# Kernel tuning notes

Hardware: AMD Instinct MI355X
Metric: run time of the kernel (lower is better)

## Reference

```python
import jax, jax.numpy as jnp
import numpy as np

B = 8192
TEXT_DIM = 2048
GRAPH_DIM = 1024
OUT_DIM = 1024
C = 2048  # common_dim = max(text_dim, graph_dim)
H = 16    # num_heads
LN_EPS = 1e-5


def _linear(x, W, b):
    # torch nn.Linear: y = x @ W.T + b, W: [out, in]
    return x @ W.T + b


def _mha(q, k, v, Wqkv, bqkv, Wo, bo):
    # Faithful to torch nn.MultiheadAttention (batch_first, eval mode).
    # Wqkv: [3C, C], bqkv: [3C], Wo: [C, C], bo: [C]
    Bq, S, _ = q.shape
    D = C // H
    Wq, Wk, Wv = Wqkv[:C], Wqkv[C:2 * C], Wqkv[2 * C:]
    bq, bk, bv = bqkv[:C], bqkv[C:2 * C], bqkv[2 * C:]
    qh = _linear(q, Wq, bq).reshape(Bq, S, H, D).transpose(0, 2, 1, 3)  # [B,H,S,D]
    kh = _linear(k, Wk, bk).reshape(Bq, S, H, D).transpose(0, 2, 1, 3)
    vh = _linear(v, Wv, bv).reshape(Bq, S, H, D).transpose(0, 2, 1, 3)
    scores = jnp.einsum('bhqd,bhkd->bhqk', qh, kh) / jnp.sqrt(jnp.asarray(D, qh.dtype))
    attn = jax.nn.softmax(scores, axis=-1)
    out = jnp.einsum('bhqk,bhkd->bhqd', attn, vh)
    out = out.transpose(0, 2, 1, 3).reshape(Bq, S, C)
    return _linear(out, Wo, bo)


def _layernorm(x, w, b):
    mu = jnp.mean(x, axis=-1, keepdims=True)
    var = jnp.mean(jnp.square(x - mu), axis=-1, keepdims=True)
    return (x - mu) * jax.lax.rsqrt(var + LN_EPS) * w + b


def setup_inputs() -> dict:
    key = jax.random.key(0)
    ks = jax.random.split(key, 16)
    s = 0.02
    return {
        'text_embeddings': jax.random.normal(ks[0], (B, TEXT_DIM), jnp.float32),
        'graph_embeddings': jax.random.normal(ks[1], (B, GRAPH_DIM), jnp.float32),
        'Wt': jax.random.normal(ks[2], (C, TEXT_DIM), jnp.float32) * s,
        'bt': jnp.zeros((C,), jnp.float32),
        'Wg': jax.random.normal(ks[3], (C, GRAPH_DIM), jnp.float32) * s,
        'bg': jnp.zeros((C,), jnp.float32),
        'Wqkv_s': jax.random.normal(ks[4], (3 * C, C), jnp.float32) * s,
        'bqkv_s': jnp.zeros((3 * C,), jnp.float32),
        'Wo_s': jax.random.normal(ks[5], (C, C), jnp.float32) * s,
        'bo_s': jnp.zeros((C,), jnp.float32),
        'Wqkv_c': jax.random.normal(ks[6], (3 * C, C), jnp.float32) * s,
        'bqkv_c': jnp.zeros((3 * C,), jnp.float32),
        'Wo_c': jax.random.normal(ks[7], (C, C), jnp.float32) * s,
        'bo_c': jnp.zeros((C,), jnp.float32),
        'ln_w': jnp.ones((C,), jnp.float32),
        'ln_b': jnp.zeros((C,), jnp.float32),
        'Wout': jax.random.normal(ks[8], (OUT_DIM, C), jnp.float32) * s,
        'bout': jnp.zeros((OUT_DIM,), jnp.float32),
    }


def reference(text_embeddings, graph_embeddings, Wt, bt, Wg, bg,
              Wqkv_s, bqkv_s, Wo_s, bo_s, Wqkv_c, bqkv_c, Wo_c, bo_c,
              ln_w, ln_b, Wout, bout):
    text_proj = _linear(text_embeddings, Wt, bt)    # [B, C]
    graph_proj = _linear(graph_embeddings, Wg, bg)  # [B, C]
    stacked = jnp.stack([text_proj, graph_proj], axis=1)  # [B, 2, C]
    attn_out = _mha(stacked, stacked, stacked, Wqkv_s, bqkv_s, Wo_s, bo_s)
    attn_out = _layernorm(attn_out, ln_w, ln_b)
    cross = _mha(attn_out, stacked, stacked, Wqkv_c, bqkv_c, Wo_c, bo_c)
    attn_out = attn_out + cross
    fused = jnp.mean(attn_out, axis=1)  # [B, C]
    return _linear(fused, Wout, bout)   # [B, OUT_DIM]
```

## Files before the change

kernel.cpp:

```cpp
#include <hip/hip_runtime.h>
#include <cstdio>

typedef unsigned short u16;
typedef float f32x4 __attribute__((ext_vector_type(4)));
typedef short s16x8 __attribute__((ext_vector_type(8)));

__device__ __forceinline__ u16 f2bf(float x) {
    unsigned u = __float_as_uint(x);
    u += 0x7fffu + ((u >> 16) & 1u);
    return (u16)(u >> 16);
}
__device__ __forceinline__ unsigned pack2(float a, float b) {
    return (unsigned)f2bf(a) | ((unsigned)f2bf(b) << 16);
}
__device__ __forceinline__ void unpack2(unsigned u, float& lo, float& hi) {
    lo = __uint_as_float(u << 16);
    hi = __uint_as_float(u & 0xffff0000u);
}

__device__ __forceinline__ void gl2lds16(const u16* g, u16* l) {
    __builtin_amdgcn_global_load_lds(
        (const __attribute__((address_space(1))) void*)g,
        (__attribute__((address_space(3))) void*)l, 16, 0, 0);
}

__device__ __forceinline__ uint4 ld8(const u16* p) { return *(const uint4*)p; }
__device__ __forceinline__ uint4 ld8(const float* p) {
    float4 a = ((const float4*)p)[0];
    float4 b = ((const float4*)p)[1];
    uint4 r;
    r.x = pack2(a.x, a.y);
    r.y = pack2(a.z, a.w);
    r.z = pack2(b.x, b.y);
    r.w = pack2(b.z, b.w);
    return r;
}

__global__ __launch_bounds__(256) void cast_f32_bf16(const float* __restrict__ x,
                                                     u16* __restrict__ y, int n4) {
    int i = blockIdx.x * 256 + threadIdx.x;
    if (i >= n4) return;
    float4 v = ((const float4*)x)[i];
    uint2 r;
    r.x = pack2(v.x, v.y);
    r.y = pack2(v.z, v.w);
    ((uint2*)y)[i] = r;
}

template <typename TA, typename TB, bool OUT_BF16>
__global__ __launch_bounds__(256) void gemm_bt(const TA* __restrict__ A,
                                               const TB* __restrict__ B,
                                               const float* __restrict__ bias,
                                               void* __restrict__ Cout,
                                               int K, int ldc) {
    __shared__ __align__(16) u16 As[128 * 32];
    __shared__ __align__(16) u16 Bs[128 * 32];

    const int tid = threadIdx.x;
    const int lane = tid & 63;
    const int wave = tid >> 6;
    const int wm = wave >> 1;
    const int wn = wave & 1;
    const size_t bm = (size_t)blockIdx.y * 128;
    const size_t bn = (size_t)blockIdx.x * 128;

    f32x4 acc[4][4];
#pragma unroll
    for (int i = 0; i < 4; ++i)
#pragma unroll
        for (int j = 0; j < 4; ++j) acc[i][j] = (f32x4)0.f;

    const int srow = tid >> 2;
    const int scol = (tid & 3) << 3;
    const TA* Ag = A + (bm + (size_t)srow) * K + scol;
    const TB* Bg = B + (bn + (size_t)srow) * K + scol;
    const size_t rstep = (size_t)64 * K;

    uint4 a0 = ld8(Ag);
    uint4 a1 = ld8(Ag + rstep);
    uint4 b0 = ld8(Bg);
    uint4 b1 = ld8(Bg + rstep);

    const int lrow = lane & 15;
    const int lk = (lane >> 4) << 3;

    const int niter = K >> 5;
    for (int t = 0; t < niter; ++t) {
        __syncthreads();
        *(uint4*)&As[srow * 32 + scol] = a0;
        *(uint4*)&As[(64 + srow) * 32 + scol] = a1;
        *(uint4*)&Bs[srow * 32 + scol] = b0;
        *(uint4*)&Bs[(64 + srow) * 32 + scol] = b1;
        __syncthreads();
        if (t + 1 < niter) {
            const int k0 = (t + 1) << 5;
            a0 = ld8(Ag + k0);
            a1 = ld8(Ag + rstep + k0);
            b0 = ld8(Bg + k0);
            b1 = ld8(Bg + rstep + k0);
        }
        s16x8 af[4], bfr[4];
#pragma unroll
        for (int i = 0; i < 4; ++i)
            af[i] = *(const s16x8*)&As[(wm * 64 + i * 16 + lrow) * 32 + lk];
#pragma unroll
        for (int j = 0; j < 4; ++j)
            bfr[j] = *(const s16x8*)&Bs[(wn * 64 + j * 16 + lrow) * 32 + lk];
#pragma unroll
        for (int i = 0; i < 4; ++i)
#pragma unroll
            for (int j = 0; j < 4; ++j)
                acc[i][j] = __builtin_amdgcn_mfma_f32_16x16x32_bf16(
                    af[i], bfr[j], acc[i][j], 0, 0, 0);
    }

    const size_t crow0 = bm + wm * 64 + ((lane >> 4) << 2);
    const int ccol0 = (int)bn + wn * 64 + (lane & 15);
#pragma unroll
    for (int i = 0; i < 4; ++i) {
#pragma unroll
        for (int j = 0; j < 4; ++j) {
            const int col = ccol0 + j * 16;
            const float bv = bias[col];
            const size_t base = (crow0 + (size_t)i * 16) * (size_t)ldc + col;
#pragma unroll
            for (int r = 0; r < 4; ++r) {
                const float v = acc[i][j][r] + bv;
                if (OUT_BF16)
                    ((u16*)Cout)[base + (size_t)r * ldc] = f2bf(v);
                else
                    ((float*)Cout)[base + (size_t)r * ldc] = v;
            }
        }
    }
}

template <bool OUT_BF16>
__global__ __launch_bounds__(256) void gemm_async(const u16* __restrict__ A, int lda,
                                                  const u16* __restrict__ B,
                                                  const float* __restrict__ bias,
                                                  void* __restrict__ Cout,
                                                  int K, int ldc) {
    __shared__ __align__(16) u16 As[128 * 32];
    __shared__ __align__(16) u16 Bs[128 * 32];

    const int tid = threadIdx.x;
    const int lane = tid & 63;
    const int wave = tid >> 6;
    const int wm = wave >> 1;
    const int wn = wave & 1;
    const size_t bm = (size_t)blockIdx.y * 128;
    const size_t bn = (size_t)blockIdx.x * 128;

    f32x4 acc[4][4];
#pragma unroll
    for (int i = 0; i < 4; ++i)
#pragma unroll
        for (int j = 0; j < 4; ++j) acc[i][j] = (f32x4)0.f;

    const int srow = tid >> 2;
    const int scol = (tid & 3) << 3;
    const u16* Ag = A + (bm + (size_t)srow) * (size_t)lda + scol;
    const u16* Bg = B + (bn + (size_t)srow) * (size_t)K + scol;
    const size_t rA = (size_t)64 * lda;
    const size_t rB = (size_t)64 * K;
    u16* lA0 = &As[tid * 8];
    u16* lA1 = &As[2048 + tid * 8];
    u16* lB0 = &Bs[tid * 8];
    u16* lB1 = &Bs[2048 + tid * 8];

    const int lrow = lane & 15;
    const int lk = (lane >> 4) << 3;

    const int niter = K >> 5;
    for (int t = 0; t < niter; ++t) {
        __syncthreads();
        gl2lds16(Ag, lA0);
        gl2lds16(Ag + rA, lA1);
        gl2lds16(Bg, lB0);
        gl2lds16(Bg + rB, lB1);
        Ag += 32;
        Bg += 32;
        __syncthreads();
        s16x8 af[4], bfr[4];
#pragma unroll
        for (int i = 0; i < 4; ++i)
            af[i] = *(const s16x8*)&As[(wm * 64 + i * 16 + lrow) * 32 + lk];
#pragma unroll
        for (int j = 0; j < 4; ++j)
            bfr[j] = *(const s16x8*)&Bs[(wn * 64 + j * 16 + lrow) * 32 + lk];
#pragma unroll
        for (int i = 0; i < 4; ++i)
#pragma unroll
            for (int j = 0; j < 4; ++j)
                acc[i][j] = __builtin_amdgcn_mfma_f32_16x16x32_bf16(
                    af[i], bfr[j], acc[i][j], 0, 0, 0);
    }

    const size_t crow0 = bm + wm * 64 + ((lane >> 4) << 2);
    const int ccol0 = (int)bn + wn * 64 + (lane & 15);
#pragma unroll
    for (int i = 0; i < 4; ++i) {
#pragma unroll
        for (int j = 0; j < 4; ++j) {
            const int col = ccol0 + j * 16;
            const float bv = bias[col];
            const size_t base = (crow0 + (size_t)i * 16) * (size_t)ldc + col;
#pragma unroll
            for (int r = 0; r < 4; ++r) {
                const float v = acc[i][j][r] + bv;
                if (OUT_BF16)
                    ((u16*)Cout)[base + (size_t)r * ldc] = f2bf(v);
                else
                    ((float*)Cout)[base + (size_t)r * ldc] = v;
            }
        }
    }
}

#define STG_A02(v)                                                            \
    do {                                                                      \
        gl2lds16(aG + (size_t)(v) * 64, &As[(v) & 1][tid * 8]);               \
        gl2lds16(aG + 2 * a64 + (size_t)(v) * 64,                             \
                 &As[(v) & 1][8192 + tid * 8]);                               \
    } while (0)
#define STG_A13(v)                                                            \
    do {                                                                      \
        gl2lds16(aG + a64 + (size_t)(v) * 64, &As[(v) & 1][4096 + tid * 8]);  \
        gl2lds16(aG + 3 * a64 + (size_t)(v) * 64,                             \
                 &As[(v) & 1][12288 + tid * 8]);                              \
    } while (0)
#define STG_B01(v)                                                            \
    do {                                                                      \
        gl2lds16(bG + (size_t)(v) * 64, &Bs[(v) & 1][tid * 8]);               \
        gl2lds16(bG + b64 + (size_t)(v) * 64, &Bs[(v) & 1][4096 + tid * 8]);  \
    } while (0)
#define STG_B23(v)                                                            \
    do {                                                                      \
        gl2lds16(bG + 2 * b64 + (size_t)(v) * 64,                             \
                 &Bs[(v) & 1][8192 + tid * 8]);                               \
        gl2lds16(bG + 3 * b64 + (size_t)(v) * 64,                             \
                 &Bs[(v) & 1][12288 + tid * 8]);                              \
    } while (0)
#define RD_AF(buf, mh, m)                                                     \
    do {                                                                      \
        const u16* p_ = &As[buf][aRow + ((mh) * 64 + (m) * 16) * 64];         \
        aF[m][0] = *(const s16x8*)(p_ + aK0);                                 \
        aF[m][1] = *(const s16x8*)(p_ + aK1);                                 \
    } while (0)
#define RD_B(buf, nh, dst)                                                    \
    do {                                                                      \
        _Pragma("unroll") for (int n_ = 0; n_ < 2; ++n_) {                    \
            const u16* p_ = &Bs[buf][bRow + ((nh) * 32 + n_ * 16) * 64];      \
            dst[n_][0] = *(const s16x8*)(p_ + aK0);                           \
            dst[n_][1] = *(const s16x8*)(p_ + aK1);                           \
        }                                                                     \
    } while (0)
#define MFMA4(ar, bv, ci, cj)                                                 \
    do {                                                                      \
        acc[ci][cj] = __builtin_amdgcn_mfma_f32_16x16x32_bf16(                \
            (ar)[0], (bv)[0], acc[ci][cj], 0, 0, 0);                          \
        acc[ci][cj] = __builtin_amdgcn_mfma_f32_16x16x32_bf16(                \
            (ar)[1], (bv)[1], acc[ci][cj], 0, 0, 0);                          \
    } while (0)

#define TILEW(u, SA13, S2, RDN, V2S, V4S)                                     \
    do {                                                                      \
        const int cur = (u) & 1, oth = cur ^ 1;                               \
                                                          \
        if (SA13) STG_A13((u) + 1);                                           \
        RD_B(cur, 1, b1);                                                     \
        __builtin_amdgcn_s_setprio(1);                                        \
        _Pragma("unroll") for (int m = 0; m < 4; ++m) {                       \
            MFMA4(aF[m], b0[0], m, 0);                                        \
            MFMA4(aF[m], b0[1], m, 1);                                        \
        }                                                                     \
        __builtin_amdgcn_s_setprio(0);                                        \
        asm volatile("s_waitcnt " V2S ::: "memory");                          \
        __builtin_amdgcn_s_barrier();                                         \
                                  \
        if (S2) STG_A02((u) + 2);                                             \
        __builtin_amdgcn_s_setprio(1);                                        \
        _Pragma("unroll") for (int m = 0; m < 4; ++m) {                       \
            MFMA4(aF[m], b1[0], m, 2);                                        \
            MFMA4(aF[m], b1[1], m, 3);                                        \
            RD_AF(cur, 1, m);                                                 \
        }                                                                     \
        __builtin_amdgcn_s_setprio(0);                                        \
        __builtin_amdgcn_s_barrier();                                         \
                                                          \
        if (S2) STG_B01((u) + 2);                                             \
        __builtin_amdgcn_s_setprio(1);                                        \
        _Pragma("unroll") for (int m = 0; m < 4; ++m) {                       \
            MFMA4(aF[m], b1[0], 4 + m, 2);                                    \
            MFMA4(aF[m], b1[1], 4 + m, 3);                                    \
        }                                                                     \
        __builtin_amdgcn_s_setprio(0);                                        \
        asm volatile("s_waitcnt " V4S ::: "memory");                          \
        __builtin_amdgcn_s_barrier();                                         \
                         \
        if (S2) STG_B23((u) + 2);                                             \
        __builtin_amdgcn_s_setprio(1);                                        \
        _Pragma("unroll") for (int m = 0; m < 4; ++m) {                       \
            MFMA4(aF[m], b0[0], 4 + m, 0);                                    \
            MFMA4(aF[m], b0[1], 4 + m, 1);                                    \
            if (RDN) RD_AF(oth, 0, m);                                        \
        }                                                                     \
        __builtin_amdgcn_s_setprio(0);                                        \
        if (RDN) RD_B(oth, 0, b0);                                            \
        __builtin_amdgcn_s_barrier();                                         \
    } while (0)

template <bool OUT_BF16>
__global__ __launch_bounds__(512, 2) void gemm8(const u16* __restrict__ A, int lda,
                                                const u16* __restrict__ B,
                                                const float* __restrict__ bias,
                                                void* __restrict__ Cout,
                                                int K, int ldc) {
    __shared__ __align__(16) u16 As[2][16384];
    __shared__ __align__(16) u16 Bs[2][16384];

    const int tid = threadIdx.x;
    const int lane = tid & 63;
    const int wave = tid >> 6;
    const int wm = wave >> 2;
    const int wn = wave & 3;

    const unsigned nwg = gridDim.x * gridDim.y;
    const unsigned orig = blockIdx.y * gridDim.x + blockIdx.x;
    const unsigned q = nwg >> 3, r = nwg & 7u;
    const unsigned xcd = orig & 7u, idx = orig >> 3;
    const unsigned wg =
        (xcd < r ? xcd * (q + 1) : r * (q + 1) + (xcd - r) * q) + idx;
    const size_t bm = (size_t)(wg / gridDim.x) * 256;
    const size_t bn = (size_t)(wg % gridDim.x) * 256;

    f32x4 acc[8][4];
#pragma unroll
    for (int i = 0; i < 8; ++i)
#pragma unroll
        for (int j = 0; j < 4; ++j) acc[i][j] = (f32x4)0.f;

    const int strow = tid >> 3;
    const int ssw = ((tid & 7) << 3) ^ ((strow & 7) << 3);
    const u16* aG = A + (bm + (size_t)strow) * (size_t)lda + ssw;
    const u16* bG = B + (bn + (size_t)strow) * (size_t)K + ssw;
    const size_t a64 = (size_t)64 * lda;
    const size_t b64 = (size_t)64 * K;

    const int lrow = lane & 15;
    const int hi8 = (lane >> 4) << 3;
    const int fswz = (lrow & 7) << 3;
    const int aK0 = hi8 ^ fswz;
    const int aK1 = (32 + hi8) ^ fswz;
    const int aRow = (wm * 128 + lrow) * 64;
    const int bRow = (wn * 64 + lrow) * 64;

    s16x8 aF[4][2], b0[2][2], b1[2][2];

    const int NT = K >> 6;

    STG_A02(0);
    STG_A13(0);
    STG_B01(0);
    STG_B23(0);
    STG_A02(1);
    STG_B01(1);
    STG_B23(1);
    asm volatile("s_waitcnt vmcnt(6)" ::: "memory");
    __builtin_amdgcn_s_barrier();
#pragma unroll
    for (int m = 0; m < 4; ++m) RD_AF(0, 0, m);
    RD_B(0, 0, b0);

    for (int u = 0; u < NT - 2; ++u)
        TILEW(u, 1, 1, 1, "vmcnt(8)", "vmcnt(6)");
    TILEW(NT - 2, 1, 0, 1, "vmcnt(8)", "vmcnt(2)");
    TILEW(NT - 1, 0, 0, 0, "vmcnt(0)", "vmcnt(0)");

    const size_t crow0 = bm + wm * 128 + ((lane >> 4) << 2);
    const int ccol0 = (int)bn + wn * 64 + (lane & 15);
#pragma unroll
    for (int im = 0; im < 8; ++im) {
#pragma unroll
        for (int in = 0; in < 4; ++in) {
            const int col = ccol0 + in * 16;
            const float bv = bias[col];
            const size_t base = (crow0 + (size_t)im * 16) * (size_t)ldc + col;
#pragma unroll
            for (int r = 0; r < 4; ++r) {
                const float v = acc[im][in][r] + bv;
                if (OUT_BF16)
                    ((u16*)Cout)[base + (size_t)r * ldc] = f2bf(v);
                else
                    ((float*)Cout)[base + (size_t)r * ldc] = v;
            }
        }
    }
}

#undef STG_A02
#undef STG_A13
#undef STG_B01
#undef STG_B23
#undef RD_AF
#undef RD_B
#undef MFMA4
#undef TILEW

__device__ __forceinline__ void dot8(uint4 a, uint4 b, float& acc) {
    const unsigned* pa = (const unsigned*)&a;
    const unsigned* pb = (const unsigned*)&b;
#pragma unroll
    for (int i = 0; i < 4; ++i) {
        float alo, ahi, blo, bhi;
        unpack2(pa[i], alo, ahi);
        unpack2(pb[i], blo, bhi);
        acc += alo * blo + ahi * bhi;
    }
}

__global__ __launch_bounds__(256) void attn2(u16* __restrict__ qkv) {
    const int gid = blockIdx.x * 256 + threadIdx.x;
    const int b = gid >> 4;
    const int h = gid & 15;
    u16* base = qkv + (size_t)(2 * b) * 6144 + h * 128;
    float s00 = 0.f, s01 = 0.f, s10 = 0.f, s11 = 0.f;
#pragma unroll 4
    for (int c = 0; c < 128; c += 8) {
        uint4 q0 = *(const uint4*)(base + c);
        uint4 q1 = *(const uint4*)(base + 6144 + c);
        uint4 k0 = *(const uint4*)(base + 2048 + c);
        uint4 k1 = *(const uint4*)(base + 8192 + c);
        dot8(q0, k0, s00);
        dot8(q0, k1, s01);
        dot8(q1, k0, s10);
        dot8(q1, k1, s11);
    }
    const float scale = 0.0883883476483184f;
    s00 *= scale; s01 *= scale; s10 *= scale; s11 *= scale;
    const float m0 = fmaxf(s00, s01), m1 = fmaxf(s10, s11);
    const float e00 = __expf(s00 - m0), e01 = __expf(s01 - m0);
    const float e10 = __expf(s10 - m1), e11 = __expf(s11 - m1);
    const float r0 = 1.f / (e00 + e01), r1 = 1.f / (e10 + e11);
    const float p00 = e00 * r0, p01 = e01 * r0;
    const float p10 = e10 * r1, p11 = e11 * r1;

#pragma unroll 4
    for (int c = 0; c < 128; c += 8) {
        uint4 v0 = *(const uint4*)(base + 4096 + c);
        uint4 v1 = *(const uint4*)(base + 10240 + c);
        const unsigned* p0w = (const unsigned*)&v0;
        const unsigned* p1w = (const unsigned*)&v1;
        uint4 r0v, r1v;
        unsigned* q0w = (unsigned*)&r0v;
        unsigned* q1w = (unsigned*)&r1v;
#pragma unroll
        for (int i = 0; i < 4; ++i) {
            float v0lo, v0hi, v1lo, v1hi;
            unpack2(p0w[i], v0lo, v0hi);
            unpack2(p1w[i], v1lo, v1hi);
            q0w[i] = pack2(p00 * v0lo + p01 * v1lo, p00 * v0hi + p01 * v1hi);
            q1w[i] = pack2(p10 * v0lo + p11 * v1lo, p10 * v0hi + p11 * v1hi);
        }
        *(uint4*)(base + c) = r0v;
        *(uint4*)(base + 6144 + c) = r1v;
    }
}

__global__ __launch_bounds__(256) void ln_k(const u16* __restrict__ x, int ldx,
                                            const float* __restrict__ w,
                                            const float* __restrict__ bb,
                                            u16* __restrict__ y) {
    __shared__ float red[8];
    const int row = blockIdx.x;
    const int tid = threadIdx.x;
    const uint4 v = ((const uint4*)(x + (size_t)row * ldx))[tid];
    const unsigned* pw = (const unsigned*)&v;
    float f[8];
#pragma unroll
    for (int i = 0; i < 4; ++i) unpack2(pw[i], f[2 * i], f[2 * i + 1]);
    float s = 0.f, q = 0.f;
#pragma unroll
    for (int i = 0; i < 8; ++i) {
        s += f[i];
        q += f[i] * f[i];
    }
#pragma unroll
    for (int off = 32; off > 0; off >>= 1) {
        s += __shfl_down(s, off);
        q += __shfl_down(q, off);
    }
    if ((tid & 63) == 0) {
        red[tid >> 6] = s;
        red[4 + (tid >> 6)] = q;
    }
    __syncthreads();
    s = red[0] + red[1] + red[2] + red[3];
    q = red[4] + red[5] + red[6] + red[7];
    const float mu = s * (1.f / 2048.f);
    const float var = q * (1.f / 2048.f) - mu * mu;
    const float rstd = rsqrtf(var + 1e-5f);
    const float4 w0 = ((const float4*)w)[2 * tid];
    const float4 w1 = ((const float4*)w)[2 * tid + 1];
    const float4 b0 = ((const float4*)bb)[2 * tid];
    const float4 b1 = ((const float4*)bb)[2 * tid + 1];
    const float wv[8] = {w0.x, w0.y, w0.z, w0.w, w1.x, w1.y, w1.z, w1.w};
    const float bv[8] = {b0.x, b0.y, b0.z, b0.w, b1.x, b1.y, b1.z, b1.w};
    uint4 o;
    unsigned* po = (unsigned*)&o;
#pragma unroll
    for (int i = 0; i < 4; ++i) {
        float lo = (f[2 * i] - mu) * rstd * wv[2 * i] + bv[2 * i];
        float hi = (f[2 * i + 1] - mu) * rstd * wv[2 * i + 1] + bv[2 * i + 1];
        po[i] = pack2(lo, hi);
    }
    ((uint4*)(y + (size_t)row * 2048))[tid] = o;
}

__global__ __launch_bounds__(256) void mean_res(const u16* __restrict__ ln,
                                                const u16* __restrict__ co,
                                                u16* __restrict__ fused) {
    const int gid = blockIdx.x * 256 + threadIdx.x;
    const int b = gid >> 8;
    const int c8 = gid & 255;
    const uint4 l0 = ((const uint4*)(ln + (size_t)(2 * b) * 2048))[c8];
    const uint4 l1 = ((const uint4*)(ln + (size_t)(2 * b + 1) * 2048))[c8];
    const uint4 c0 = ((const uint4*)(co + (size_t)(2 * b) * 6144))[c8];
    const uint4 c1 = ((const uint4*)(co + (size_t)(2 * b + 1) * 6144))[c8];
    const unsigned* pl0 = (const unsigned*)&l0;
    const unsigned* pl1 = (const unsigned*)&l1;
    const unsigned* pc0 = (const unsigned*)&c0;
    const unsigned* pc1 = (const unsigned*)&c1;
    uint4 o;
    unsigned* po = (unsigned*)&o;
#pragma unroll
    for (int i = 0; i < 4; ++i) {
        float a_lo, a_hi, b_lo, b_hi, c_lo, c_hi, d_lo, d_hi;
        unpack2(pl0[i], a_lo, a_hi);
        unpack2(pl1[i], b_lo, b_hi);
        unpack2(pc0[i], c_lo, c_hi);
        unpack2(pc1[i], d_lo, d_hi);
        po[i] = pack2(0.5f * (a_lo + c_lo + b_lo + d_lo),
                      0.5f * (a_hi + c_hi + b_hi + d_hi));
    }
    ((uint4*)(fused + (size_t)b * 12288))[c8] = o;
}

extern "C" void kernel_launch(void* const* d_in, const int* in_sizes, int n_in,
                              void* d_out, int out_size, void* d_ws, size_t ws_size,
                              hipStream_t stream) {
    (void)in_sizes; (void)n_in; (void)out_size;
    const float* text   = (const float*)d_in[0];
    const float* graph  = (const float*)d_in[1];
    const float* Wt     = (const float*)d_in[2];
    const float* bt     = (const float*)d_in[3];
    const float* Wg     = (const float*)d_in[4];
    const float* bg     = (const float*)d_in[5];
    const float* Wqkv_s = (const float*)d_in[6];
    const float* bqkv_s = (const float*)d_in[7];
    const float* Wo_s   = (const float*)d_in[8];
    const float* bo_s   = (const float*)d_in[9];
    const float* Wqkv_c = (const float*)d_in[10];
    const float* bqkv_c = (const float*)d_in[11];
    const float* Wo_c   = (const float*)d_in[12];
    const float* bo_c   = (const float*)d_in[13];
    const float* ln_w   = (const float*)d_in[14];
    const float* ln_b   = (const float*)d_in[15];
    const float* Wout   = (const float*)d_in[16];
    const float* bout   = (const float*)d_in[17];
    float* out = (float*)d_out;

    char* ws = (char*)d_ws;
    u16* wQs  = (u16*)ws;
    u16* wQc  = wQs + 12582912ull;
    u16* wOs  = wQc + 12582912ull;
    u16* wOc  = wOs + 4194304ull;
    u16* wWt  = wOc + 4194304ull;
    u16* wWg  = wWt + 4194304ull;
    u16* wOut = wWg + 2097152ull;
    const size_t WB = 83886080ull;

    size_t CH = 8192;
    while (CH > 128 && WB + 40960ull * CH > ws_size) CH >>= 1;
    fprintf(stderr, "[kernel_launch] ws_size=%zu need=%zu CH=%zu\n",
            ws_size, WB + 40960ull * CH, CH);
    if (WB + 40960ull * CH > ws_size || d_ws == nullptr) return;

    const size_t T = 2 * CH;
    char* ca = ws + WB;
    u16* stacked_c = (u16*)ca;
    u16* ln_c      = (u16*)(ca + 4096 * T);
    u16* qkv_c     = (u16*)(ca + 8192 * T);

    auto cast = [&](const float* x, u16* y, size_t n) {
        int n4 = (int)(n >> 2);
        cast_f32_bf16<<<(n4 + 255) / 256, 256, 0, stream>>>(x, y, n4);
    };
    cast(Wqkv_s, wQs, 12582912ull);
    cast(Wqkv_c, wQc, 12582912ull);
    cast(Wo_s, wOs, 4194304ull);
    cast(Wo_c, wOc, 4194304ull);
    cast(Wt, wWt, 4194304ull);
    cast(Wg, wWg, 2097152ull);
    cast(Wout, wOut, 2097152ull);

    const dim3 blk(256);
    const dim3 blk8(512);
    const unsigned gy  = (unsigned)(CH / 128);
    const unsigned g8  = (unsigned)(T / 256);

    for (size_t c0 = 0; c0 < 8192; c0 += CH) {
        gemm_bt<float, u16, true><<<dim3(16, gy), blk, 0, stream>>>(
            text + c0 * 2048, wWt, bt, stacked_c, 2048, 4096);
        gemm_bt<float, u16, true><<<dim3(16, gy), blk, 0, stream>>>(
            graph + c0 * 1024, wWg, bg, stacked_c + 2048, 1024, 4096);
        gemm8<true><<<dim3(24, g8), blk8, 0, stream>>>(
            stacked_c, 2048, wQs, bqkv_s, qkv_c, 2048, 6144);
        attn2<<<(unsigned)(CH / 16), blk, 0, stream>>>(qkv_c);
        gemm8<true><<<dim3(8, g8), blk8, 0, stream>>>(
            qkv_c, 6144, wOs, bo_s, qkv_c + 4096, 2048, 6144);
        ln_k<<<(unsigned)T, blk, 0, stream>>>(qkv_c + 4096, 6144, ln_w, ln_b, ln_c);
        gemm8<true><<<dim3(8, g8), blk8, 0, stream>>>(
            ln_c, 2048, wQc, bqkv_c, qkv_c, 2048, 6144);
        gemm8<true><<<dim3(16, g8), blk8, 0, stream>>>(
            stacked_c, 2048, wQc + 2048ull * 2048, bqkv_c + 2048,
            qkv_c + 2048, 2048, 6144);
        attn2<<<(unsigned)(CH / 16), blk, 0, stream>>>(qkv_c);
        gemm8<true><<<dim3(8, g8), blk8, 0, stream>>>(
            qkv_c, 6144, wOc, bo_c, qkv_c + 4096, 2048, 6144);
        mean_res<<<(unsigned)CH, blk, 0, stream>>>(ln_c, qkv_c + 4096, qkv_c);
        gemm_async<false><<<dim3(8, gy), blk, 0, stream>>>(
            qkv_c, 12288, wOut, bout, out + c0 * 1024, 2048, 1024);
    }
}
```

Before: 1.955 ms.

## Restructure GEMM main loop into four barrier-separated LDS-read/MFMA phases

Replaces the interleaved TILEW schedule, which overlapped LDS fragment reads with MFMAs and prefetched the next tile's fragments, with a TILE4 scheme. Each of the four quadrants now reads its fragments, waits on lgkmcnt(0), then runs its MFMAs behind sched_barriers. Global-to-LDS staging of A is moved to only one tile ahead and the prologue stages less up front. The aim is to simplify the schedule and cut dependence stalls. The cost is that LDS read latency is no longer hidden behind MFMAs and there are more barriers per tile.

```diff
diff --git a/kernel.cpp b/kernel.cpp
--- a/kernel.cpp
+++ b/kernel.cpp
@@ -256,58 +256,56 @@
             dst[n_][1] = *(const s16x8*)(p_ + aK1);                           \
         }                                                                     \
     } while (0)
-#define MFMA4(ar, bv, ci, cj)                                                 \
-    do {                                                                      \
-        acc[ci][cj] = __builtin_amdgcn_mfma_f32_16x16x32_bf16(                \
-            (ar)[0], (bv)[0], acc[ci][cj], 0, 0, 0);                          \
-        acc[ci][cj] = __builtin_amdgcn_mfma_f32_16x16x32_bf16(                \
-            (ar)[1], (bv)[1], acc[ci][cj], 0, 0, 0);                          \
-    } while (0)
-
-#define TILEW(u, SA13, S2, RDN, V2S, V4S)                                     \
-    do {                                                                      \
-        const int cur = (u) & 1, oth = cur ^ 1;                               \
-                                                          \
-        if (SA13) STG_A13((u) + 1);                                           \
-        RD_B(cur, 1, b1);                                                     \
+#define MFMA_Q(mh, nh, bf)                                                    \
+    do {                                                                      \
         __builtin_amdgcn_s_setprio(1);                                        \
-        _Pragma("unroll") for (int m = 0; m < 4; ++m) {                       \
-            MFMA4(aF[m], b0[0], m, 0);                                        \
-            MFMA4(aF[m], b0[1], m, 1);                                        \
+        _Pragma("unroll") for (int m = 0; m < 4; ++m)                         \
+            _Pragma("unroll") for (int n = 0; n < 2; ++n) {                   \
+            acc[(mh)*4 + m][(nh)*2 + n] =                                     \
+                __builtin_amdgcn_mfma_f32_16x16x32_bf16(                      \
+                    aF[m][0], bf[n][0], acc[(mh)*4 + m][(nh)*2 + n], 0, 0, 0);\
+            acc[(mh)*4 + m][(nh)*2 + n] =                                     \
+                __builtin_amdgcn_mfma_f32_16x16x32_bf16(                      \
+                    aF[m][1], bf[n][1], acc[(mh)*4 + m][(nh)*2 + n], 0, 0, 0);\
         }                                                                     \
         __builtin_amdgcn_s_setprio(0);                                        \
-        asm volatile("s_waitcnt " V2S ::: "memory");                          \
-        __builtin_amdgcn_s_barrier();                                         \
-                                  \
-        if (S2) STG_A02((u) + 2);                                             \
-        __builtin_amdgcn_s_setprio(1);                                        \
-        _Pragma("unroll") for (int m = 0; m < 4; ++m) {                       \
-            MFMA4(aF[m], b1[0], m, 2);                                        \
-            MFMA4(aF[m], b1[1], m, 3);                                        \
-            RD_AF(cur, 1, m);                                                 \
-        }                                                                     \
-        __builtin_amdgcn_s_setprio(0);                                        \
-        __builtin_amdgcn_s_barrier();                                         \
-                                                          \
-        if (S2) STG_B01((u) + 2);                                             \
-        __builtin_amdgcn_s_setprio(1);                                        \
-        _Pragma("unroll") for (int m = 0; m < 4; ++m) {                       \
-            MFMA4(aF[m], b1[0], 4 + m, 2);                                    \
-            MFMA4(aF[m], b1[1], 4 + m, 3);                                    \
-        }                                                                     \
-        __builtin_amdgcn_s_setprio(0);                                        \
-        asm volatile("s_waitcnt " V4S ::: "memory");                          \
-        __builtin_amdgcn_s_barrier();                                         \
-                         \
-        if (S2) STG_B23((u) + 2);                                             \
-        __builtin_amdgcn_s_setprio(1);                                        \
-        _Pragma("unroll") for (int m = 0; m < 4; ++m) {                       \
-            MFMA4(aF[m], b0[0], 4 + m, 0);                                    \
-            MFMA4(aF[m], b0[1], 4 + m, 1);                                    \
-            if (RDN) RD_AF(oth, 0, m);                                        \
-        }                                                                     \
-        __builtin_amdgcn_s_setprio(0);                                        \
-        if (RDN) RD_B(oth, 0, b0);                                            \
+    } while (0)
+
+#define TILE4(u, DO_A, DO_B, W2S, W4S)                                        \
+    do {                                                                      \
+        const int cur = (u) & 1;                                              \
+                                                                      \
+        _Pragma("unroll") for (int m = 0; m < 4; ++m) RD_AF(cur, 0, m);       \
+        RD_B(cur, 0, b0);                                                     \
+        if (DO_A) STG_A02((u) + 1);                                           \
+        __builtin_amdgcn_s_barrier();                                         \
+        asm volatile("s_waitcnt lgkmcnt(0)" ::: "memory");                    \
+        __builtin_amdgcn_sched_barrier(0);                                    \
+        MFMA_Q(0, 0, b0);                                                     \
+        __builtin_amdgcn_s_barrier();                                         \
+                                                                      \
+        RD_B(cur, 1, b1);                                                     \
+        if (DO_A) STG_A13((u) + 1);                                           \
+        __builtin_amdgcn_s_barrier();                                         \
+        asm volatile("s_waitcnt lgkmcnt(0)" ::: "memory");                    \
+        __builtin_amdgcn_sched_barrier(0);                                    \
+        MFMA_Q(0, 1, b1);                                                     \
+        asm volatile("s_waitcnt " W2S ::: "memory");                          \
+        __builtin_amdgcn_s_barrier();                                         \
+                                                                      \
+        _Pragma("unroll") for (int m = 0; m < 4; ++m) RD_AF(cur, 1, m);       \
+        if (DO_B) STG_B01((u) + 2);                                           \
+        __builtin_amdgcn_s_barrier();                                         \
+        asm volatile("s_waitcnt lgkmcnt(0)" ::: "memory");                    \
+        __builtin_amdgcn_sched_barrier(0);                                    \
+        MFMA_Q(1, 1, b1);                                                     \
+        __builtin_amdgcn_s_barrier();                                         \
+                                                                      \
+        if (DO_B) STG_B23((u) + 2);                                           \
+        __builtin_amdgcn_s_barrier();                                         \
+        __builtin_amdgcn_sched_barrier(0);                                    \
+        MFMA_Q(1, 0, b0);                                                     \
+        asm volatile("s_waitcnt " W4S ::: "memory");                          \
         __builtin_amdgcn_s_barrier();                                         \
     } while (0)
 
@@ -364,19 +362,15 @@
     STG_A13(0);
     STG_B01(0);
     STG_B23(0);
-    STG_A02(1);
     STG_B01(1);
     STG_B23(1);
-    asm volatile("s_waitcnt vmcnt(6)" ::: "memory");
+    asm volatile("s_waitcnt vmcnt(4)" ::: "memory");
     __builtin_amdgcn_s_barrier();
-#pragma unroll
-    for (int m = 0; m < 4; ++m) RD_AF(0, 0, m);
-    RD_B(0, 0, b0);
 
     for (int u = 0; u < NT - 2; ++u)
-        TILEW(u, 1, 1, 1, "vmcnt(8)", "vmcnt(6)");
-    TILEW(NT - 2, 1, 0, 1, "vmcnt(8)", "vmcnt(2)");
-    TILEW(NT - 1, 0, 0, 0, "vmcnt(0)", "vmcnt(0)");
+        TILE4(u, 1, 1, "vmcnt(8)", "vmcnt(6)");
+    TILE4(NT - 2, 1, 0, "vmcnt(8)", "vmcnt(2)");
+    TILE4(NT - 1, 0, 0, "vmcnt(0)", "vmcnt(0)");
 
     const size_t crow0 = bm + wm * 128 + ((lane >> 4) << 2);
     const int ccol0 = (int)bn + wn * 64 + (lane & 15);
@@ -405,8 +399,8 @@
 #undef STG_B23
 #undef RD_AF
 #undef RD_B
-#undef MFMA4
-#undef TILEW
+#undef MFMA_Q
+#undef TILE4
 
 __device__ __forceinline__ void dot8(uint4 a, uint4 b, float& acc) {
     const unsigned* pa = (const unsigned*)&a;
```

New measurement: 2.075 ms. 1.06x slower.
